# Kernel tuning notes

Hardware: AMD Instinct MI355X
Metric: run time of the kernel (lower is better)

Reference implementation:

```python
import jax, jax.numpy as jnp
import numpy as np

H = 8
D = 512
DK = D // H  # 64
ALPHA = 0.2  # leaky relu negative slope


def setup_inputs() -> dict:
    key = jax.random.key(0)
    ks = jax.random.split(key, 10)
    B, N = 8, 1024
    query = jax.random.normal(ks[0], (B, N, D), dtype=jnp.float32)
    key_t = jax.random.normal(ks[1], (B, N, D), dtype=jnp.float32)
    value = jax.random.normal(ks[2], (B, N, D), dtype=jnp.float32)
    mask = jax.random.randint(ks[3], (B, N, N), 0, 2, dtype=jnp.int32)
    scale = 0.02
    Wq = jax.random.normal(ks[4], (D, D), dtype=jnp.float32) * scale
    Wk = jax.random.normal(ks[5], (D, D), dtype=jnp.float32) * scale
    Wv = jax.random.normal(ks[6], (D, D), dtype=jnp.float32) * scale
    Wo = jax.random.normal(ks[7], (D, D), dtype=jnp.float32) * scale
    bq = jnp.zeros((D,), jnp.float32)
    bk = jnp.zeros((D,), jnp.float32)
    bv = jnp.zeros((D,), jnp.float32)
    bo = jnp.zeros((D,), jnp.float32)
    # xavier-uniform-like init for the attention vector a: shape (h, 2*d_k)
    limit = float(np.sqrt(6.0 / (H + 2 * DK)))
    a = jax.random.uniform(ks[8], (H, 2 * DK), dtype=jnp.float32, minval=-limit, maxval=limit)
    return {"query": query, "key": key_t, "value": value, "mask": mask,
            "Wq": Wq, "bq": bq, "Wk": Wk, "bk": bk, "Wv": Wv, "bv": bv,
            "Wo": Wo, "bo": bo, "a": a}


def reference(query, key, value, mask, Wq, bq, Wk, bk, Wv, bv, Wo, bo, a):
    B, N, _ = query.shape

    def proj(x, W, b):
        # torch Linear: x @ W.T + b, then split heads -> (B, H, N, DK)
        return (x @ W.T + b).reshape(B, N, H, DK).transpose(0, 2, 1, 3)

    q = proj(query, Wq, bq)
    k = proj(key, Wk, bk)
    v = proj(value, Wv, bv)

    # 'cat' attention: scores[b,h,i,j] = concat(q_i, k_j) . a[h]
    #                = q_i . a[h,:DK] + k_j . a[h,DK:]  (algebraic decomposition,
    #                 avoids the O(N^2 * 2*DK) concat tensor of the torch code)
    sq = jnp.einsum('bhnd,hd->bhn', q, a[:, :DK])
    sk = jnp.einsum('bhnd,hd->bhn', k, a[:, DK:])
    scores = sq[:, :, :, None] + sk[:, :, None, :]  # (B, H, N, N)

    # mask == 0 -> -inf (mask broadcast over heads), applied BEFORE leaky relu
    scores = jnp.where(mask[:, None, :, :] == 0, -jnp.inf, scores)
    # leaky relu (leaky_relu(-inf) == -inf, preserved)
    scores = jnp.where(scores >= 0, scores, ALPHA * scores)

    p = jax.nn.softmax(scores, axis=-1)
    # fully-masked rows produce NaN -> replace with 0 (as in the torch code)
    p = jnp.where(jnp.isnan(p), jnp.zeros_like(p), p)

    x = jnp.einsum('bhnm,bhmd->bhnd', p, v)
    x = x.transpose(0, 2, 1, 3).reshape(B, N, D)
    return x @ Wo.T + bo
```

## Files before the change

kernel.cpp:

```cpp
#include <hip/hip_runtime.h>
#include <hip/hip_bf16.h>
#include <stdint.h>


typedef __attribute__((ext_vector_type(8))) short short8;
typedef __attribute__((ext_vector_type(4))) float f32x4;

#define LB __launch_bounds__(256)

union U8 { unsigned u[4]; short8 s; uint4 v; };
union U2 { unsigned u[2]; uint2 v; };

__device__ __forceinline__ unsigned short f2bf(float f) {
  unsigned int u = __float_as_uint(f);
  u += 0x7fffu + ((u >> 16) & 1u);
  return (unsigned short)(u >> 16);
}

__device__ __forceinline__ unsigned cvt_pk(float a, float b) {
  unsigned r;
  asm("v_cvt_pk_bf16_f32 %0, %1, %2" : "=v"(r) : "v"(a), "v"(b));
  return r;
}

__device__ __forceinline__ void async_cp16(const void* g, void* l) {
  __builtin_amdgcn_global_load_lds(
      (const __attribute__((address_space(1))) unsigned int*)g,
      (__attribute__((address_space(3))) unsigned int*)l, 16, 0, 0);
}

__global__ LB void prep_kernel(const float* __restrict__ Wv, const float* __restrict__ Wo,
                               unsigned short* __restrict__ wv16, unsigned short* __restrict__ wo16,
                               const float* __restrict__ Wq, const float* __restrict__ Wk,
                               const float* __restrict__ a, const float* __restrict__ bq,
                               const float* __restrict__ bk,
                               unsigned short* __restrict__ Bfrag, float* __restrict__ qkb) {
  const int blk = blockIdx.x, tid = threadIdx.x;
  if (blk < 512) {
    const float* src = blk < 256 ? Wv : Wo;
    unsigned short* dst = blk < 256 ? wv16 : wo16;
    const int idx = ((blk & 255) * 256 + tid) * 4;
    const float4 v = *(const float4*)(src + idx);
    U2 pk;
    pk.u[0] = cvt_pk(v.x, v.y);
    pk.u[1] = cvt_pk(v.z, v.w);
    *(uint2*)(dst + idx) = pk.v;
    return;
  }
  const int t = (blk - 512) * 256 + tid;
  const int d = t & 511, h = t >> 9;
  float aq = 0.f, ak = 0.f;
#pragma unroll 4
  for (int dk = 0; dk < 64; ++dk) {
    aq += Wq[(size_t)(h * 64 + dk) * 512 + d] * a[h * 128 + dk];
    ak += Wk[(size_t)(h * 64 + dk) * 512 + d] * a[h * 128 + 64 + dk];
  }
  const float L2E = 1.4426950408889634f;
  const int ks = d >> 5, lch = (d >> 3) & 3, tt = d & 7;
  Bfrag[((ks * 64 + (lch << 4) + h) << 3) + tt] = f2bf(aq * L2E);
  Bfrag[((ks * 64 + (lch << 4) + 8 + h) << 3) + tt] = f2bf(ak * L2E);
  if (d == 0) {
    float s1 = 0.f, s2 = 0.f;
    for (int dk = 0; dk < 64; ++dk) {
      s1 += bq[h * 64 + dk] * a[h * 128 + dk];
      s2 += bk[h * 64 + dk] * a[h * 128 + 64 + dk];
    }
    qkb[h] = s1 * L2E;
    qkb[8 + h] = s2 * L2E;
  }
}

__global__ LB void mid_kernel(const float* __restrict__ query, const float* __restrict__ key,
                              const unsigned short* __restrict__ Bfrag,
                              const float* __restrict__ qkb,
                              float* __restrict__ sq, float* __restrict__ sk,
                              const float* __restrict__ value,
                              const unsigned short* __restrict__ wv16,
                              const float* __restrict__ bvb, unsigned short* __restrict__ vt,
                              const int* __restrict__ mask, unsigned int* __restrict__ bits) {
  __shared__ char sm[20480];
  const int tid = threadIdx.x, w = tid >> 6, l = tid & 63;
  const int lr = l & 15, lc = l >> 4;
  const int bid = blockIdx.x;
  if (bid >= 1536) {
    unsigned char* nb = (unsigned char*)sm;
    const size_t e0 = ((size_t)(bid - 1536) * 256 + tid) * 4;
    const int4 m = *(const int4*)(mask + e0);
    nb[tid] = (unsigned char)((m.x != 0) | ((m.y != 0) << 1) | ((m.z != 0) << 2) | ((m.w != 0) << 3));
    __syncthreads();
    if (tid < 32) {
      const uint2 p = *(const uint2*)(nb + tid * 8);
      const unsigned lo = p.x, hi = p.y;
      const unsigned wl = (lo & 0xFu) | ((lo >> 4) & 0xF0u) | ((lo >> 8) & 0xF00u) | ((lo >> 12) & 0xF000u);
      const unsigned wh = (hi & 0xFu) | ((hi >> 4) & 0xF0u) | ((hi >> 8) & 0xF00u) | ((hi >> 12) & 0xF000u);
      bits[(bid - 1536) * 32 + tid] = wl | (wh << 16);
    }
    return;
  }
  if (bid >= 1024) {
    float* comb = (float*)sm;
    const int m0 = (bid - 1024) * 16;
    const int k0 = w * 128;
    short8 bf[4];
#pragma unroll
    for (int ks = 0; ks < 4; ++ks)
      bf[ks] = *(const short8*)(Bfrag + (((w * 4 + ks) * 64 + l) << 3));
    const float* qbase = query + (size_t)(m0 + lr) * 512 + k0 + (lc << 3);
    const float* kbase = key + (size_t)(m0 + lr) * 512 + k0 + (lc << 3);
    f32x4 cq = {}, ck = {};
#pragma unroll
    for (int ks = 0; ks < 4; ++ks) {
      const float4 q0 = *(const float4*)(qbase + ks * 32);
      const float4 q1 = *(const float4*)(qbase + ks * 32 + 4);
      const float4 k0v = *(const float4*)(kbase + ks * 32);
      const float4 k1v = *(const float4*)(kbase + ks * 32 + 4);
      U8 aq, ak;
      aq.u[0] = cvt_pk(q0.x, q0.y); aq.u[1] = cvt_pk(q0.z, q0.w);
      aq.u[2] = cvt_pk(q1.x, q1.y); aq.u[3] = cvt_pk(q1.z, q1.w);
      ak.u[0] = cvt_pk(k0v.x, k0v.y); ak.u[1] = cvt_pk(k0v.z, k0v.w);
      ak.u[2] = cvt_pk(k1v.x, k1v.y); ak.u[3] = cvt_pk(k1v.z, k1v.w);
      cq = __builtin_amdgcn_mfma_f32_16x16x32_bf16(aq.s, bf[ks], cq, 0, 0, 0);
      ck = __builtin_amdgcn_mfma_f32_16x16x32_bf16(ak.s, bf[ks], ck, 0, 0, 0);
    }
    if (w) {
      float* p = comb + ((w - 1) * 64 + l) * 9;
#pragma unroll
      for (int r = 0; r < 4; ++r) { p[r] = cq[r]; p[4 + r] = ck[r]; }
    }
    __syncthreads();
    if (w == 0) {
#pragma unroll
      for (int j = 0; j < 3; ++j) {
        const float* p = comb + (j * 64 + l) * 9;
#pragma unroll
        for (int r = 0; r < 4; ++r) { cq[r] += p[r]; ck[r] += p[4 + r]; }
      }
      const int col = l & 15;
      const int mbase = m0 + (lc << 2);
      const int b = mbase >> 10;
      const float bia = qkb[col];
      if (col < 8) {
        float* out = sq + ((size_t)b * 8 + col) * 1024;
#pragma unroll
        for (int r = 0; r < 4; ++r) out[(mbase + r) & 1023] = cq[r] + bia;
      } else {
        float* out = sk + ((size_t)b * 8 + (col - 8)) * 1024;
#pragma unroll
        for (int r = 0; r < 4; ++r) out[(mbase + r) & 1023] = ck[r] + bia;
      }
    }
    return;
  }
  unsigned short* As = (unsigned short*)sm;
  unsigned short* Bs = (unsigned short*)(sm + 4096);
  const int bm = bid >> 2, bn = bid & 3;
  const int m0 = bm * 32, n0 = bn * 128;
  const int wr = (w & 1) * 16, wc = (w >> 1) * 64;
  const int rch = (lc ^ ((lr >> 1) & 3)) << 3;
  const int arow = (w << 3) + (l >> 3);
  const int akc = l & 7;
  const float* asrc = value + (size_t)(m0 + arow) * 512 + (akc << 2);
  const int ach = ((akc >> 1) ^ ((arow >> 1) & 3));
  const int aoff = arow * 32 + (ach << 3) + ((akc & 1) << 2);
  const int crow = l >> 2;
  const int brow0 = (w << 4) + crow, brow1 = ((w + 4) << 4) + crow;
  const unsigned short* bsrc0 = wv16 + (size_t)(n0 + brow0) * 512 + (((l & 3) ^ ((brow0 >> 1) & 3)) << 3);
  const unsigned short* bsrc1 = wv16 + (size_t)(n0 + brow1) * 512 + (((l & 3) ^ ((brow1 >> 1) & 3)) << 3);

  f32x4 acc[4] = {};
  float4 areg = *(const float4*)(asrc);
  async_cp16(bsrc0, Bs + (w << 9));
  async_cp16(bsrc1, Bs + ((w + 4) << 9));
  {
    U2 aw;
    aw.u[0] = cvt_pk(areg.x, areg.y);
    aw.u[1] = cvt_pk(areg.z, areg.w);
    *(uint2*)(As + aoff) = aw.v;
  }
  areg = *(const float4*)(asrc + 32);
  async_cp16(bsrc0 + 32, Bs + 4096 + (w << 9));
  async_cp16(bsrc1 + 32, Bs + 4096 + ((w + 4) << 9));
  asm volatile("s_waitcnt vmcnt(3)" ::: "memory");
  asm volatile("s_waitcnt lgkmcnt(0)" ::: "memory");
  __builtin_amdgcn_sched_barrier(0);
  __builtin_amdgcn_s_barrier();
  int buf = 0;
  for (int kt = 0; kt < 16; ++kt) {
    const short8 af = *(const short8*)(As + (buf << 10) + (wr + lr) * 32 + rch);
    __builtin_amdgcn_s_setprio(1);
#pragma unroll
    for (int j = 0; j < 4; ++j) {
      const short8 bfr = *(const short8*)(Bs + (buf << 12) + (wc + j * 16 + lr) * 32 + rch);
      acc[j] = __builtin_amdgcn_mfma_f32_16x16x32_bf16(af, bfr, acc[j], 0, 0, 0);
    }
    __builtin_amdgcn_s_setprio(0);
    __builtin_amdgcn_s_barrier();
    if (kt < 15) {
      U2 aw;
      aw.u[0] = cvt_pk(areg.x, areg.y);
      aw.u[1] = cvt_pk(areg.z, areg.w);
      *(uint2*)(As + ((buf ^ 1) << 10) + aoff) = aw.v;
      if (kt < 14) {
        areg = *(const float4*)(asrc + (kt + 2) * 32);
        async_cp16(bsrc0 + (kt + 2) * 32, Bs + (buf << 12) + (w << 9));
        async_cp16(bsrc1 + (kt + 2) * 32, Bs + (buf << 12) + ((w + 4) << 9));
        asm volatile("s_waitcnt vmcnt(3)" ::: "memory");
      } else {
        asm volatile("s_waitcnt vmcnt(0)" ::: "memory");
      }
      asm volatile("s_waitcnt lgkmcnt(0)" ::: "memory");
      __builtin_amdgcn_sched_barrier(0);
      __builtin_amdgcn_s_barrier();
    }
    buf ^= 1;
  }
#pragma unroll
  for (int j = 0; j < 4; ++j) {
    const int nn = n0 + wc + j * 16 + lr;
    const float bia = bvb[nn];
    const int mm0 = m0 + wr + lc * 4;
    const int b = mm0 >> 10, t0 = mm0 & 1023;
    const int h = nn >> 6, dk = nn & 63;
    U2 pk;
    pk.u[0] = cvt_pk(acc[j][0] + bia, acc[j][1] + bia);
    pk.u[1] = cvt_pk(acc[j][2] + bia, acc[j][3] + bia);
    *(uint2*)(vt + (((size_t)((b * 8 + h) * 64 + dk)) << 10) + t0) = pk.v;
  }
}

template <int BB16>
__global__ LB void gemm_bt(const unsigned short* __restrict__ A,
                           const void* __restrict__ Bwp,
                           const float* __restrict__ bias, float* __restrict__ outp) {
  __shared__ unsigned short As[2][32 * 32];
  __shared__ unsigned short Bs[2][128 * 32];
  const int tid = threadIdx.x;
  const int w = tid >> 6, l = tid & 63;
  const int lr = l & 15, lc = l >> 4;
  const int bm = blockIdx.x >> 2, bn = blockIdx.x & 3;
  const int m0 = bm * 32, n0 = bn * 128;
  const int wr = (w & 1) * 16, wc = (w >> 1) * 64;
  const int rch = (lc ^ ((lr >> 1) & 3)) << 3;
  const int arow = (w << 3) + (l >> 2);
  const int asc = (l & 3) ^ ((arow >> 1) & 3);
  const unsigned short* asrc = A + (size_t)(m0 + arow) * 512 + (asc << 3);
  const int crow = l >> 2;
  const unsigned short* b16 = (const unsigned short*)Bwp;
  const float* b32 = (const float*)Bwp;
  const int brow0 = (w << 4) + crow, brow1 = ((w + 4) << 4) + crow;
  const unsigned short* bsrc0 = b16 + (size_t)(n0 + brow0) * 512 + (((l & 3) ^ ((brow0 >> 1) & 3)) << 3);
  const unsigned short* bsrc1 = b16 + (size_t)(n0 + brow1) * 512 + (((l & 3) ^ ((brow1 >> 1) & 3)) << 3);

  f32x4 acc[4] = {};
  if (BB16) {
    if (l < 32) async_cp16(asrc, As[0] + (w << 8));
    async_cp16(bsrc0, Bs[0] + (w << 9));
    async_cp16(bsrc1, Bs[0] + ((w + 4) << 9));
    int buf = 0;
    for (int kt = 0; kt < 16; ++kt) {
      if (kt < 15) {
        const int k1 = (kt + 1) * 32;
        if (l < 32) async_cp16(asrc + k1, As[buf ^ 1] + (w << 8));
        async_cp16(bsrc0 + k1, Bs[buf ^ 1] + (w << 9));
        async_cp16(bsrc1 + k1, Bs[buf ^ 1] + ((w + 4) << 9));
        asm volatile("s_waitcnt vmcnt(3)" ::: "memory");
      } else {
        asm volatile("s_waitcnt vmcnt(0)" ::: "memory");
      }
      __builtin_amdgcn_sched_barrier(0);
      __builtin_amdgcn_s_barrier();
      const short8 af = *(const short8*)(As[buf] + (wr + lr) * 32 + rch);
      __builtin_amdgcn_s_setprio(1);
#pragma unroll
      for (int j = 0; j < 4; ++j) {
        const short8 bfr = *(const short8*)(Bs[buf] + (wc + j * 16 + lr) * 32 + rch);
        acc[j] = __builtin_amdgcn_mfma_f32_16x16x32_bf16(af, bfr, acc[j], 0, 0, 0);
      }
      __builtin_amdgcn_s_setprio(0);
      if (kt < 15) __builtin_amdgcn_s_barrier();
      buf ^= 1;
    }
  } else {
    for (int kt = 0; kt < 16; ++kt) {
      const int k0 = kt * 32;
      if (kt) __syncthreads();
      if (l < 32) async_cp16(asrc + k0, As[0] + (w << 8));
#pragma unroll
      for (int it = 0; it < 2; ++it) {
        const int idx = it * 256 + tid;
        const int row = idx >> 2, gr = idx & 3;
        const int sch = (gr ^ ((row >> 1) & 3)) << 3;
        const float4* src = (const float4*)(b32 + (size_t)(n0 + row) * 512 + k0 + gr * 8);
        const float4 b0 = src[0], b1 = src[1];
        U8 t8;
        t8.u[0] = cvt_pk(b0.x, b0.y); t8.u[1] = cvt_pk(b0.z, b0.w);
        t8.u[2] = cvt_pk(b1.x, b1.y); t8.u[3] = cvt_pk(b1.z, b1.w);
        *(uint4*)(Bs[0] + row * 32 + sch) = t8.v;
      }
      __syncthreads();
      const short8 af = *(const short8*)(As[0] + (wr + lr) * 32 + rch);
#pragma unroll
      for (int j = 0; j < 4; ++j) {
        const short8 bfr = *(const short8*)(Bs[0] + (wc + j * 16 + lr) * 32 + rch);
        acc[j] = __builtin_amdgcn_mfma_f32_16x16x32_bf16(af, bfr, acc[j], 0, 0, 0);
      }
    }
  }
#pragma unroll
  for (int j = 0; j < 4; ++j) {
    const int nn = n0 + wc + j * 16 + lr;
    const float bia = bias[nn];
    const int mm0 = m0 + wr + lc * 4;
#pragma unroll
    for (int r = 0; r < 4; ++r)
      outp[(size_t)(mm0 + r) * 512 + nn] = acc[j][r] + bia;
  }
}

__global__ LB void attn_kernel(const float* __restrict__ sq, const float* __restrict__ sk,
                               const unsigned char* __restrict__ mbits,
                               const unsigned short* __restrict__ vt,
                               unsigned short* __restrict__ xb) {
  __shared__ char smem[45056];
  unsigned short* vts = (unsigned short*)smem;
  float* sks = (float*)(smem + 32768);
  char* mks = smem + 36864;
  const int tid = threadIdx.x;
  const int w = tid >> 6, l = tid & 63;
  const int lr = l & 15, lc = l >> 4;
  const int bid = blockIdx.x;
  const int bh = bid & 63, iblk = bid >> 6;
  const int b = bh >> 3, h = bh & 7;
  const int i0b = iblk << 6;
  const int j0 = w << 8;
  const float* sqp = sq + (size_t)bh * 1024;
  const float* skp = sk + (size_t)bh * 1024;
  const unsigned short* vtp = vt + ((size_t)bh << 16);
  const unsigned char* mrow = mbits + ((size_t)b << 17);

  async_cp16(skp + (w << 8) + l * 4, sks + (w << 8));
#pragma unroll
  for (int m = 0; m < 2; ++m) {
    const int row = (w << 4) + (m << 3) + (l >> 3);
    const int c = (l & 7) ^ (row & 7);
    async_cp16(mrow + (size_t)(i0b + row) * 128 + (c << 4), mks + (w << 11) + (m << 10));
  }
  const int stl = l >> 2;
  const int stc = (l & 3) ^ ((stl >> 1) & 3);
  const unsigned short* vsrc = vtp + stl * 1024 + j0 + (stc << 3);
#define STAGE(bf_, jb_)                                                        \
  {                                                                            \
    unsigned short* d_ = vts + (w << 12) + ((bf_) << 11);                      \
    const unsigned short* s_ = vsrc + (jb_);                                   \
    async_cp16(s_, d_);                                                        \
    async_cp16(s_ + 16384, d_ + 512);                                          \
    async_cp16(s_ + 32768, d_ + 1024);                                         \
    async_cp16(s_ + 49152, d_ + 1536);                                         \
  }
  STAGE(0, 0);
  float sq8[4];
#pragma unroll
  for (int t = 0; t < 4; ++t) sq8[t] = sqp[i0b + (t << 4) + lr];
  __syncthreads();

  f32x4 acc[4][4] = {};
  f32x4 accs[4] = {};
  short8 ones;
#pragma unroll
  for (int t = 0; t < 8; ++t) ones[t] = (short)0x3f80;
  const int rx = (lr & 7) << 4;
  const int vread = (lc ^ ((lr >> 1) & 3)) << 3;

  int buf = 0;
  for (int s = 0; s < 8; ++s) {
    if (s < 7) {
      STAGE(buf ^ 1, (s + 1) << 5);
      asm volatile("s_waitcnt vmcnt(4)" ::: "memory");
    } else {
      asm volatile("s_waitcnt vmcnt(0)" ::: "memory");
    }
    __builtin_amdgcn_sched_barrier(0);
    const int jb = j0 + (s << 5);
    const int qb = (jb >> 3) + lc;
    const f32x4 s0 = *(const f32x4*)(sks + jb + (lc << 3));
    const f32x4 s1 = *(const f32x4*)(sks + jb + (lc << 3) + 4);
    U8 pa[4];
#pragma unroll
    for (int t = 0; t < 4; ++t) {
      const int row = (t << 4) + lr;
      const unsigned mb = (unsigned char)mks[(row << 7) + (qb ^ rx)];
      const float sqv = sq8[t];
      float e[8];
#pragma unroll
      for (int u = 0; u < 8; ++u) {
        float sv = sqv + (u < 4 ? s0[u] : s1[u - 4]);
        sv = fmaxf(sv, 0.2f * sv);
        const float ex = __builtin_amdgcn_exp2f(sv);
        e[u] = (mb & (1u << u)) ? ex : 0.0f;
      }
      pa[t].u[0] = cvt_pk(e[0], e[1]); pa[t].u[1] = cvt_pk(e[2], e[3]);
      pa[t].u[2] = cvt_pk(e[4], e[5]); pa[t].u[3] = cvt_pk(e[6], e[7]);
    }
    const unsigned short* vbb = vts + (w << 12) + (buf << 11) + vread;
    __builtin_amdgcn_s_setprio(1);
#pragma unroll
    for (int c = 0; c < 4; ++c) {
      const short8 bv = *(const short8*)(vbb + ((c << 4) + lr) * 32);
#pragma unroll
      for (int t = 0; t < 4; ++t)
        acc[t][c] = __builtin_amdgcn_mfma_f32_16x16x32_bf16(pa[t].s, bv, acc[t][c], 0, 0, 0);
    }
#pragma unroll
    for (int t = 0; t < 4; ++t)
      accs[t] = __builtin_amdgcn_mfma_f32_16x16x32_bf16(pa[t].s, ones, accs[t], 0, 0, 0);
    __builtin_amdgcn_s_setprio(0);
    buf ^= 1;
  }
#undef STAGE

  __syncthreads();
  float* cmb = (float*)smem;
#define CMB_W(B_)                                                              \
  {                                                                            \
    float* p = cmb + ((B_) * 64 + l) * 85;                                     \
    _Pragma("unroll") for (int t = 0; t < 4; ++t) {                            \
      _Pragma("unroll") for (int c = 0; c < 4; ++c)                            \
          *(f32x4*)(p + (t * 4 + c) * 4) = acc[t][c];                          \
      *(f32x4*)(p + 64 + t * 4) = accs[t];                                     \
    }                                                                          \
  }
#define CMB_A(B_)                                                              \
  {                                                                            \
    const float* p = cmb + ((B_) * 64 + l) * 85;                               \
    _Pragma("unroll") for (int t = 0; t < 4; ++t) {                            \
      _Pragma("unroll") for (int c = 0; c < 4; ++c) {                          \
        const f32x4 v = *(const f32x4*)(p + (t * 4 + c) * 4);                  \
        _Pragma("unroll") for (int r = 0; r < 4; ++r) acc[t][c][r] += v[r];    \
      }                                                                        \
      const f32x4 vs = *(const f32x4*)(p + 64 + t * 4);                        \
      _Pragma("unroll") for (int r = 0; r < 4; ++r) accs[t][r] += vs[r];       \
    }                                                                          \
  }
  if (w == 1) CMB_W(0);
  if (w == 3) CMB_W(1);
  __syncthreads();
  if (w == 0) CMB_A(0);
  if (w == 2) CMB_A(1);
  __syncthreads();
  if (w == 2) CMB_W(0);
  __syncthreads();
  if (w == 0) {
    CMB_A(0);
#pragma unroll
    for (int t = 0; t < 4; ++t) {
#pragma unroll
      for (int r = 0; r < 4; ++r) {
        const float sv = accs[t][r];
        const float inv = sv > 0.0f ? 1.0f / sv : 0.0f;
        const int i = i0b + (t << 4) + (lc << 2) + r;
#pragma unroll
        for (int c = 0; c < 4; ++c)
          xb[(((size_t)(b * 1024 + i)) << 9) + h * 64 + (c << 4) + lr] =
              f2bf(acc[t][c][r] * inv);
      }
    }
  }
#undef CMB_W
#undef CMB_A
}

extern "C" void kernel_launch(void* const* d_in, const int* in_sizes, int n_in,
                              void* d_out, int out_size, void* d_ws, size_t ws_size,
                              hipStream_t stream) {
  const float* query = (const float*)d_in[0];
  const float* key   = (const float*)d_in[1];
  const float* value = (const float*)d_in[2];
  const int*   mask  = (const int*)d_in[3];
  const float* Wq = (const float*)d_in[4];
  const float* bq = (const float*)d_in[5];
  const float* Wk = (const float*)d_in[6];
  const float* bk = (const float*)d_in[7];
  const float* Wv = (const float*)d_in[8];
  const float* bv = (const float*)d_in[9];
  const float* Wo = (const float*)d_in[10];
  const float* bo = (const float*)d_in[11];
  const float* a  = (const float*)d_in[12];

  char* oc = (char*)d_out;
  unsigned short* vt = (unsigned short*)(oc + 0);
  unsigned int* mbits = (unsigned int*)(oc + 8388608);
  float* sqv = (float*)(oc + 9437184);
  float* skv = (float*)(oc + 9699328);
  unsigned short* Bfrag = (unsigned short*)(oc + 9961472);
  float* qkb = (float*)(oc + 9977856);
  unsigned short* wv16 = (unsigned short*)(oc + 10485760);
  unsigned short* xb = (unsigned short*)d_ws;

  const bool roomy = ws_size >= 8912896;
  unsigned short* wo16 = roomy ? (unsigned short*)((char*)d_ws + 8388608) : (unsigned short*)(oc + 11010048);

  prep_kernel<<<528, 256, 0, stream>>>(Wv, Wo, wv16, wo16, Wq, Wk, a, bq, bk, Bfrag, qkb);
  mid_kernel<<<9728, 256, 0, stream>>>(query, key, Bfrag, qkb, sqv, skv,
                                       value, wv16, bv, vt, mask, mbits);
  attn_kernel<<<1024, 256, 0, stream>>>(sqv, skv, (const unsigned char*)mbits, vt, xb);
  if (roomy)
    gemm_bt<1><<<1024, 256, 0, stream>>>(xb, (const void*)wo16, bo, (float*)d_out);
  else
    gemm_bt<0><<<1024, 256, 0, stream>>>(xb, (const void*)Wo, bo, (float*)d_out);
}
```

Baseline: 90.86 us.

## Double attention block rows to 128 with 8 waves sharing staged V tiles

The attention kernel now runs 512-thread blocks covering 128 query rows instead of 64. Pairs of waves share the same key range, so each staged V tile in LDS is used for two row halves, and the per-wave async copy count halves. The cost is extra block-wide barriers inside the pipelined loop, a three-round serial cross-wave reduction, larger shared memory, and half as many blocks.

```diff
diff --git a/kernel.cpp b/kernel.cpp
--- a/kernel.cpp
+++ b/kernel.cpp
@@ -7,6 +7,7 @@
 typedef __attribute__((ext_vector_type(4))) float f32x4;
 
 #define LB __launch_bounds__(256)
+#define LB512 __launch_bounds__(512)
 
 union U8 { unsigned u[4]; short8 s; uint4 v; };
 union U2 { unsigned u[2]; uint2 v; };
@@ -317,11 +318,11 @@
   }
 }
 
-__global__ LB void attn_kernel(const float* __restrict__ sq, const float* __restrict__ sk,
-                               const unsigned char* __restrict__ mbits,
-                               const unsigned short* __restrict__ vt,
-                               unsigned short* __restrict__ xb) {
-  __shared__ char smem[45056];
+__global__ LB512 void attn_kernel(const float* __restrict__ sq, const float* __restrict__ sk,
+                                  const unsigned char* __restrict__ mbits,
+                                  const unsigned short* __restrict__ vt,
+                                  unsigned short* __restrict__ xb) {
+  __shared__ char smem[53248];
   unsigned short* vts = (unsigned short*)smem;
   float* sks = (float*)(smem + 32768);
   char* mks = smem + 36864;
@@ -331,14 +332,15 @@
   const int bid = blockIdx.x;
   const int bh = bid & 63, iblk = bid >> 6;
   const int b = bh >> 3, h = bh & 7;
-  const int i0b = iblk << 6;
-  const int j0 = w << 8;
+  const int i0b = iblk << 7;
+  const int rh = w & 1, jq = w >> 1;
+  const int j0 = jq << 8;
   const float* sqp = sq + (size_t)bh * 1024;
   const float* skp = sk + (size_t)bh * 1024;
   const unsigned short* vtp = vt + ((size_t)bh << 16);
   const unsigned char* mrow = mbits + ((size_t)b << 17);
 
-  async_cp16(skp + (w << 8) + l * 4, sks + (w << 8));
+  if (w < 4) async_cp16(skp + (w << 8) + l * 4, sks + (w << 8));
 #pragma unroll
   for (int m = 0; m < 2; ++m) {
     const int row = (w << 4) + (m << 3) + (l >> 3);
@@ -346,21 +348,19 @@
     async_cp16(mrow + (size_t)(i0b + row) * 128 + (c << 4), mks + (w << 11) + (m << 10));
   }
   const int stl = l >> 2;
-  const int stc = (l & 3) ^ ((stl >> 1) & 3);
-  const unsigned short* vsrc = vtp + stl * 1024 + j0 + (stc << 3);
+  const int stc = (l & 3) ^ ((l >> 3) & 3);
+  const unsigned short* vsrc0 = vtp + (size_t)((rh << 5) + stl) * 1024 + j0 + (stc << 3);
+  const unsigned short* vsrc1 = vsrc0 + (16 << 10);
+  unsigned short* vdst = vts + (jq << 12) + (rh << 10);
 #define STAGE(bf_, jb_)                                                        \
   {                                                                            \
-    unsigned short* d_ = vts + (w << 12) + ((bf_) << 11);                      \
-    const unsigned short* s_ = vsrc + (jb_);                                   \
-    async_cp16(s_, d_);                                                        \
-    async_cp16(s_ + 16384, d_ + 512);                                          \
-    async_cp16(s_ + 32768, d_ + 1024);                                         \
-    async_cp16(s_ + 49152, d_ + 1536);                                         \
+    async_cp16(vsrc0 + (jb_), vdst + ((bf_) << 11));                           \
+    async_cp16(vsrc1 + (jb_), vdst + ((bf_) << 11) + 512);                     \
   }
   STAGE(0, 0);
   float sq8[4];
 #pragma unroll
-  for (int t = 0; t < 4; ++t) sq8[t] = sqp[i0b + (t << 4) + lr];
+  for (int t = 0; t < 4; ++t) sq8[t] = sqp[i0b + (rh << 6) + (t << 4) + lr];
   __syncthreads();
 
   f32x4 acc[4][4] = {};
@@ -375,11 +375,12 @@
   for (int s = 0; s < 8; ++s) {
     if (s < 7) {
       STAGE(buf ^ 1, (s + 1) << 5);
-      asm volatile("s_waitcnt vmcnt(4)" ::: "memory");
+      asm volatile("s_waitcnt vmcnt(2)" ::: "memory");
     } else {
       asm volatile("s_waitcnt vmcnt(0)" ::: "memory");
     }
     __builtin_amdgcn_sched_barrier(0);
+    __builtin_amdgcn_s_barrier();
     const int jb = j0 + (s << 5);
     const int qb = (jb >> 3) + lc;
     const f32x4 s0 = *(const f32x4*)(sks + jb + (lc << 3));
@@ -387,7 +388,7 @@
     U8 pa[4];
 #pragma unroll
     for (int t = 0; t < 4; ++t) {
-      const int row = (t << 4) + lr;
+      const int row = (rh << 6) + (t << 4) + lr;
       const unsigned mb = (unsigned char)mks[(row << 7) + (qb ^ rx)];
       const float sqv = sq8[t];
       float e[8];
@@ -401,7 +402,7 @@
       pa[t].u[0] = cvt_pk(e[0], e[1]); pa[t].u[1] = cvt_pk(e[2], e[3]);
       pa[t].u[2] = cvt_pk(e[4], e[5]); pa[t].u[3] = cvt_pk(e[6], e[7]);
     }
-    const unsigned short* vbb = vts + (w << 12) + (buf << 11) + vread;
+    const unsigned short* vbb = vts + (jq << 12) + (buf << 11) + vread;
     __builtin_amdgcn_s_setprio(1);
 #pragma unroll
     for (int c = 0; c < 4; ++c) {
@@ -414,24 +415,25 @@
     for (int t = 0; t < 4; ++t)
       accs[t] = __builtin_amdgcn_mfma_f32_16x16x32_bf16(pa[t].s, ones, accs[t], 0, 0, 0);
     __builtin_amdgcn_s_setprio(0);
+    if (s < 7) __builtin_amdgcn_s_barrier();
     buf ^= 1;
   }
 #undef STAGE
 
   __syncthreads();
   float* cmb = (float*)smem;
-#define CMB_W(B_)                                                              \
+#define CMB_W                                                                  \
   {                                                                            \
-    float* p = cmb + ((B_) * 64 + l) * 85;                                     \
+    float* p = cmb + ((rh << 6) + l) * 85;                                     \
     _Pragma("unroll") for (int t = 0; t < 4; ++t) {                            \
       _Pragma("unroll") for (int c = 0; c < 4; ++c)                            \
           *(f32x4*)(p + (t * 4 + c) * 4) = acc[t][c];                          \
       *(f32x4*)(p + 64 + t * 4) = accs[t];                                     \
     }                                                                          \
   }
-#define CMB_A(B_)                                                              \
+#define CMB_A                                                                  \
   {                                                                            \
-    const float* p = cmb + ((B_) * 64 + l) * 85;                               \
+    const float* p = cmb + ((rh << 6) + l) * 85;                               \
     _Pragma("unroll") for (int t = 0; t < 4; ++t) {                            \
       _Pragma("unroll") for (int c = 0; c < 4; ++c) {                          \
         const f32x4 v = *(const f32x4*)(p + (t * 4 + c) * 4);                  \
@@ -441,23 +443,21 @@
       _Pragma("unroll") for (int r = 0; r < 4; ++r) accs[t][r] += vs[r];       \
     }                                                                          \
   }
-  if (w == 1) CMB_W(0);
-  if (w == 3) CMB_W(1);
-  __syncthreads();
-  if (w == 0) CMB_A(0);
-  if (w == 2) CMB_A(1);
-  __syncthreads();
-  if (w == 2) CMB_W(0);
-  __syncthreads();
-  if (w == 0) {
-    CMB_A(0);
+#pragma unroll
+  for (int rnd = 1; rnd < 4; ++rnd) {
+    if (jq == rnd) CMB_W;
+    __syncthreads();
+    if (jq == 0) CMB_A;
+    if (rnd < 3) __syncthreads();
+  }
+  if (jq == 0) {
 #pragma unroll
     for (int t = 0; t < 4; ++t) {
 #pragma unroll
       for (int r = 0; r < 4; ++r) {
         const float sv = accs[t][r];
         const float inv = sv > 0.0f ? 1.0f / sv : 0.0f;
-        const int i = i0b + (t << 4) + (lc << 2) + r;
+        const int i = i0b + (rh << 6) + (t << 4) + (lc << 2) + r;
 #pragma unroll
         for (int c = 0; c < 4; ++c)
           xb[(((size_t)(b * 1024 + i)) << 9) + h * 64 + (c << 4) + lr] =
@@ -502,7 +502,7 @@
   prep_kernel<<<528, 256, 0, stream>>>(Wv, Wo, wv16, wo16, Wq, Wk, a, bq, bk, Bfrag, qkb);
   mid_kernel<<<9728, 256, 0, stream>>>(query, key, Bfrag, qkb, sqv, skv,
                                        value, wv16, bv, vt, mask, mbits);
-  attn_kernel<<<1024, 256, 0, stream>>>(sqv, skv, (const unsigned char*)mbits, vt, xb);
+  attn_kernel<<<512, 512, 0, stream>>>(sqv, skv, (const unsigned char*)mbits, vt, xb);
   if (roomy)
     gemm_bt<1><<<1024, 256, 0, stream>>>(xb, (const void*)wo16, bo, (float*)d_out);
   else
```

Result: no change. 92.66 us (+2.0%).
